# Optimization experiments

Hardware: AMD Instinct MI355X
Metric: run time of the kernel (lower is better)

The kernel has to match this reference:

```python
import jax, jax.numpy as jnp
import numpy as np

VOCAB = 32000
HIDDEN = 1024


def setup_inputs() -> dict:
    key = jax.random.key(0)
    k1, k2, k3 = jax.random.split(key, 3)
    inputs = jax.random.randint(k1, (4, 4096), 0, VOCAB, dtype=jnp.int64 if jax.config.jax_enable_x64 else jnp.int32)
    W0 = jax.random.normal(k2, (VOCAB, 2 * HIDDEN), dtype=jnp.float32)
    W1 = jax.random.normal(k3, (2 * HIDDEN, HIDDEN), dtype=jnp.float32)
    return {"inputs": inputs, "W0": W0, "W1": W1}


def reference(inputs, W0, W1):
    # Original builds one-hot [N, V] and does two GEMMs; mathematically this is
    # a gather of W0 rows followed by a matmul with W1.
    x = W0[inputs]                      # [B, L, 2H]  (== one_hot @ W0)
    emb = jnp.einsum('blk,kh->blh', x, W1)  # [B, L, H]
    mask = (inputs != 0).astype(emb.dtype)  # zero out padding token 0
    emb = emb * mask[..., None]
    emb = emb * jnp.asarray(HIDDEN ** 0.5, emb.dtype)
    return emb
```

## Files before the change

kernel.cpp:

```cpp
#include <hip/hip_runtime.h>
#include <stdint.h>

#define VOCAB 32000
#define KDIM  2048
#define NDIM  1024
#define MTOK  16384

typedef __bf16 bf16x8  __attribute__((ext_vector_type(8)));
typedef float  f32x4   __attribute__((ext_vector_type(4)));
typedef float  f32x16  __attribute__((ext_vector_type(16)));

__device__ __forceinline__ uint32_t pkbf(float a, float b) {
    union { __bf16 h[2]; uint32_t u; } r;
    r.h[0] = (__bf16)a; r.h[1] = (__bf16)b;
    return r.u;
}

__device__ __forceinline__ unsigned short f2bf(float f) {
    union { float f; uint32_t u; } v; v.f = f;
    uint32_t u = v.u;
    return (unsigned short)((u + 0x7FFFu + ((u >> 16) & 1u)) >> 16);
}

__device__ __forceinline__ void gload_lds16(const void* g, void* l) {
    __builtin_amdgcn_global_load_lds(
        (const __attribute__((address_space(1))) uint32_t*)g,
        (__attribute__((address_space(3))) uint32_t*)l,
        16, 0, 0);
}

__global__ void w1_transpose_kernel(const float* __restrict__ W1,
                                    unsigned short* __restrict__ W1T) {
    __shared__ unsigned short tile[32][33];
    const int k0 = blockIdx.x * 32;
    const int n0 = blockIdx.y * 32;
    const int tx = threadIdx.x;
    const int ty = threadIdx.y;
#pragma unroll
    for (int i = 0; i < 4; ++i) {
        int kl = ty + i * 8;
        tile[kl][tx] = __builtin_bit_cast(unsigned short,
                            (__bf16)W1[(size_t)(k0 + kl) * NDIM + n0 + tx]);
    }
    __syncthreads();
#pragma unroll
    for (int i = 0; i < 4; ++i) {
        int nl = ty + i * 8;
        W1T[(size_t)(n0 + nl) * KDIM + k0 + tx] = tile[tx][nl];
    }
}

__global__ __launch_bounds__(512, 2)
void emb_gemm_ws(const int* __restrict__ idx,
                 const float* __restrict__ W0,
                 const unsigned short* __restrict__ W1T,
                 float* __restrict__ out) {
    __shared__ __align__(16) char Abuf[2][256 * 128];
    __shared__ __align__(16) char Bbuf[2][256 * 128];

    const int tid  = threadIdx.x;
    const int lane = tid & 63;
    const int wav  = tid >> 6;
    const int wm   = wav >> 2;
    const int wn   = wav & 3;
    const int m0   = blockIdx.x * 256;
    const int n0   = blockIdx.y * 256;

    const int ac = tid & 15;
    uint32_t aoff[8];
    int abyte[8];
#pragma unroll
    for (int it = 0; it < 8; ++it) {
        const int r = (tid >> 4) + it * 32;
        aoff[it]  = ((uint32_t)idx[m0 + r] * KDIM + ac * 4) * 4u;
        abyte[it] = (r * 128 + ac * 8) ^ ((r & 7) << 4);
    }

    const int brin = lane >> 3;
    const int bch  = (lane & 7) ^ brin;
    uint32_t boff[4];
    int bbase[4];
#pragma unroll
    for (int i = 0; i < 4; ++i) {
        const int rg = wav * 32 + i * 8;
        boff[i]  = ((uint32_t)(n0 + rg + brin) * KDIM + bch * 8) * 2u;
        bbase[i] = rg * 128;
    }

    f32x4  apre[8];
    f32x16 acc[4][2] = {};
    bf16x8 bfv[2];

#define ISSUE_A(t)                                                   \
    _Pragma("unroll")                                                \
    for (int it = 0; it < 8; ++it)                                   \
        apre[it] = *(const f32x4*)((const char*)W0 + aoff[it] + (t) * 256);

#define WRITE_A(buf)                                                 \
    _Pragma("unroll")                                                \
    for (int it = 0; it < 8; ++it) {                                 \
        uint2 pk;                                                    \
        pk.x = pkbf(apre[it][0], apre[it][1]);                       \
        pk.y = pkbf(apre[it][2], apre[it][3]);                       \
        *(uint2*)(Abuf[buf] + abyte[it]) = pk;                       \
    }

#define ISSUE_B(buf, t)                                              \
    _Pragma("unroll")                                                \
    for (int i = 0; i < 4; ++i)                                      \
        gload_lds16((const char*)W1T + boff[i] + (t) * 128,          \
                    Bbuf[buf] + bbase[i]);

    const int rl31 = lane & 31;
    const int khi  = (lane >> 5) * 16;

#define READ_AB(buf, ks, af)                                         \
    _Pragma("unroll")                                                \
    for (int mb = 0; mb < 4; ++mb) {                                 \
        const int r = wm * 128 + mb * 32 + rl31;                     \
        af[mb] = *(const bf16x8*)(Abuf[buf] +                        \
            ((r * 128 + (ks) * 32 + khi) ^ ((r & 7) << 4)));         \
    }                                                                \
    _Pragma("unroll")                                                \
    for (int nb = 0; nb < 2; ++nb) {                                 \
        const int n = wn * 64 + nb * 32 + rl31;                      \
        bfv[nb] = *(const bf16x8*)(Bbuf[buf] +                       \
            ((n * 128 + (ks) * 32 + khi) ^ ((n & 7) << 4)));         \
    }

#define MFMA8(af)                                                    \
    __builtin_amdgcn_s_setprio(1);                                   \
    _Pragma("unroll")                                                \
    for (int mb = 0; mb < 4; ++mb)                                   \
        _Pragma("unroll")                                            \
        for (int nb = 0; nb < 2; ++nb)                               \
            acc[mb][nb] = __builtin_amdgcn_mfma_f32_32x32x16_bf16(   \
                af[mb], bfv[nb], acc[mb][nb], 0, 0, 0);              \
    __builtin_amdgcn_s_setprio(0);

    ISSUE_B(0, 0);
    ISSUE_A(0);
    WRITE_A(0);
    __syncthreads();

    for (int t = 0; t < 32; ++t) {
        const int cur = t & 1, nxt = cur ^ 1;
        const bool pf = (t < 31);
        bf16x8 af[4];

        READ_AB(cur, 0, af);
        if (pf) { ISSUE_B(nxt, t + 1); ISSUE_A(t + 1); }
        __builtin_amdgcn_s_barrier();
        MFMA8(af);
        __builtin_amdgcn_s_barrier();

        READ_AB(cur, 1, af);
        __builtin_amdgcn_s_barrier();
        MFMA8(af);
        __builtin_amdgcn_s_barrier();

        READ_AB(cur, 2, af);
        __builtin_amdgcn_s_barrier();
        MFMA8(af);
        __builtin_amdgcn_s_barrier();

        READ_AB(cur, 3, af);
        if (pf) { WRITE_A(nxt); }
        __builtin_amdgcn_s_barrier();
        MFMA8(af);
        __syncthreads();
    }

    const int hi4 = (lane >> 5) * 4;
#pragma unroll
    for (int mb = 0; mb < 4; ++mb) {
#pragma unroll
        for (int q = 0; q < 4; ++q) {
#pragma unroll
            for (int rs = 0; rs < 4; ++rs) {
                const int reg = q * 4 + rs;
                const int m = m0 + wm * 128 + mb * 32 + q * 8 + rs + hi4;
                const float msk = (idx[m] != 0) ? 32.0f : 0.0f;
#pragma unroll
                for (int nb = 0; nb < 2; ++nb) {
                    const int n = n0 + wn * 64 + nb * 32 + rl31;
                    out[(size_t)m * NDIM + n] = acc[mb][nb][reg] * msk;
                }
            }
        }
    }
#undef ISSUE_A
#undef WRITE_A
#undef ISSUE_B
#undef READ_AB
#undef MFMA8
}

__global__ __launch_bounds__(256)
void emb_gemm_nows(const int* __restrict__ idx,
                   const float* __restrict__ W0,
                   const float* __restrict__ W1,
                   float* __restrict__ out) {
    __shared__ __align__(16) char A_lds[128 * 128];
    __shared__ __align__(16) char B_lds[128 * 128];

    const int tid  = threadIdx.x;
    const int lane = tid & 63;
    const int wav  = tid >> 6;
    const int wm = wav >> 1;
    const int wn = wav & 1;
    const int m0 = blockIdx.x * 128;
    const int n0 = blockIdx.y * 128;

    const float* aSrc[8];
    int arow[8];
#pragma unroll
    for (int it = 0; it < 8; ++it) {
        int r = it * 16 + (tid >> 4);
        arow[it] = r;
        aSrc[it] = W0 + (size_t)idx[m0 + r] * KDIM;
    }
    const int acol4 = tid & 15;

    f32x4 acc[4][4] = {};

    for (int k0 = 0; k0 < KDIM; k0 += 64) {
#pragma unroll
        for (int it = 0; it < 8; ++it) {
            const int r = arow[it];
            const float4 v = *(const float4*)(aSrc[it] + k0 + acol4 * 4);
            uint2 pk;
            pk.x = pkbf(v.x, v.y);
            pk.y = pkbf(v.z, v.w);
            *(uint2*)(A_lds + ((r * 128 + acol4 * 8) ^ ((r & 7) << 4))) = pk;
        }
#pragma unroll
        for (int it = 0; it < 8; ++it) {
            const int k  = it * 8 + (tid >> 5);
            const int n4 = (tid & 31) * 4;
            const float4 v = *(const float4*)(W1 + (size_t)(k0 + k) * NDIM + n0 + n4);
            unsigned short h[4] = { f2bf(v.x), f2bf(v.y), f2bf(v.z), f2bf(v.w) };
#pragma unroll
            for (int i = 0; i < 4; ++i) {
                const int n = n4 + i;
                *(unsigned short*)(B_lds + ((n * 128 + k * 2) ^ ((n & 7) << 4))) = h[i];
            }
        }
        __syncthreads();

#pragma unroll
        for (int ks = 0; ks < 2; ++ks) {
            const int kb = ks * 64 + (lane >> 4) * 16;
            bf16x8 af[4], bfv[4];
#pragma unroll
            for (int mi = 0; mi < 4; ++mi) {
                const int r = wm * 64 + mi * 16 + (lane & 15);
                af[mi] = *(const bf16x8*)(A_lds + ((r * 128 + kb) ^ ((r & 7) << 4)));
            }
#pragma unroll
            for (int ni = 0; ni < 4; ++ni) {
                const int n = wn * 64 + ni * 16 + (lane & 15);
                bfv[ni] = *(const bf16x8*)(B_lds + ((n * 128 + kb) ^ ((n & 7) << 4)));
            }
#pragma unroll
            for (int mi = 0; mi < 4; ++mi)
#pragma unroll
                for (int ni = 0; ni < 4; ++ni)
                    acc[mi][ni] = __builtin_amdgcn_mfma_f32_16x16x32_bf16(
                        af[mi], bfv[ni], acc[mi][ni], 0, 0, 0);
        }
        __syncthreads();
    }

    const int col  = lane & 15;
    const int rowq = (lane >> 4) * 4;
#pragma unroll
    for (int mi = 0; mi < 4; ++mi) {
#pragma unroll
        for (int r = 0; r < 4; ++r) {
            const int m = m0 + wm * 64 + mi * 16 + rowq + r;
            const float msk = (idx[m] != 0) ? 32.0f : 0.0f;
#pragma unroll
            for (int ni = 0; ni < 4; ++ni) {
                const int n = n0 + wn * 64 + ni * 16 + col;
                out[(size_t)m * NDIM + n] = acc[mi][ni][r] * msk;
            }
        }
    }
}

extern "C" void kernel_launch(void* const* d_in, const int* in_sizes, int n_in,
                              void* d_out, int out_size, void* d_ws, size_t ws_size,
                              hipStream_t stream) {
    const int*   idx = (const int*)d_in[0];
    const float* W0  = (const float*)d_in[1];
    const float* W1  = (const float*)d_in[2];
    float*       out = (float*)d_out;

    const size_t w1t_bytes = (size_t)KDIM * NDIM * 2;

    if (ws_size >= w1t_bytes) {
        unsigned short* W1T = (unsigned short*)d_ws;
        dim3 tgrid(KDIM / 32, NDIM / 32);
        w1_transpose_kernel<<<tgrid, dim3(32, 8), 0, stream>>>(W1, W1T);
        dim3 grid(MTOK / 256, NDIM / 256);
        emb_gemm_ws<<<grid, 512, 0, stream>>>(idx, W0, W1T, out);
    } else {
        dim3 grid(MTOK / 128, NDIM / 128);
        emb_gemm_nows<<<grid, 256, 0, stream>>>(idx, W0, W1, out);
    }
}
```

Measured before the change: 101.2 us.

## Switch to 16x16x32 MFMA with register double-buffered LDS fragment reads

Replaces the 32x32x16 MFMA tiling with 16x16x32 bf16 MFMAs arranged as an 8x4 accumulator grid per wave, splitting each K-tile into two 64-wide K steps and two M halves. Fragment reads from LDS are ping-ponged between two register sets so the next set loads while the current MFMAs run, and the next tile's first fragments are prefetched after the barrier. This aims to hide LDS read latency and cut the number of barrier phases per tile, at the cost of more fragment registers and a changed epilogue layout.

```diff
diff --git a/kernel.cpp b/kernel.cpp
--- a/kernel.cpp
+++ b/kernel.cpp
@@ -6,9 +6,8 @@
 #define NDIM  1024
 #define MTOK  16384
 
-typedef __bf16 bf16x8  __attribute__((ext_vector_type(8)));
-typedef float  f32x4   __attribute__((ext_vector_type(4)));
-typedef float  f32x16  __attribute__((ext_vector_type(16)));
+typedef __bf16 bf16x8 __attribute__((ext_vector_type(8)));
+typedef float  f32x4  __attribute__((ext_vector_type(4)));
 
 __device__ __forceinline__ uint32_t pkbf(float a, float b) {
     union { __bf16 h[2]; uint32_t u; } r;
@@ -87,9 +86,12 @@
         bbase[i] = rg * 128;
     }
 
-    f32x4  apre[8];
-    f32x16 acc[4][2] = {};
-    bf16x8 bfv[2];
+    f32x4 apre[8];
+    f32x4 acc[8][4] = {};
+    bf16x8 afX[4], afY[4], bfX[4], bfY[4];
+
+    const int rl = lane & 15;
+    const int kq = (lane >> 4) * 16;
 
 #define ISSUE_A(t)                                                   \
     _Pragma("unroll")                                                \
@@ -111,89 +113,90 @@
         gload_lds16((const char*)W1T + boff[i] + (t) * 128,          \
                     Bbuf[buf] + bbase[i]);
 
-    const int rl31 = lane & 31;
-    const int khi  = (lane >> 5) * 16;
-
-#define READ_AB(buf, ks, af)                                         \
-    _Pragma("unroll")                                                \
-    for (int mb = 0; mb < 4; ++mb) {                                 \
-        const int r = wm * 128 + mb * 32 + rl31;                     \
-        af[mb] = *(const bf16x8*)(Abuf[buf] +                        \
-            ((r * 128 + (ks) * 32 + khi) ^ ((r & 7) << 4)));         \
-    }                                                                \
-    _Pragma("unroll")                                                \
-    for (int nb = 0; nb < 2; ++nb) {                                 \
-        const int n = wn * 64 + nb * 32 + rl31;                      \
-        bfv[nb] = *(const bf16x8*)(Bbuf[buf] +                       \
-            ((n * 128 + (ks) * 32 + khi) ^ ((n & 7) << 4)));         \
-    }
-
-#define MFMA8(af)                                                    \
+#define READ_A(buf, ks, mh, dst)                                     \
+    _Pragma("unroll")                                                \
+    for (int mi = 0; mi < 4; ++mi) {                                 \
+        const int r = wm * 128 + (mh) * 64 + mi * 16 + rl;           \
+        dst[mi] = *(const bf16x8*)(Abuf[buf] +                       \
+            ((r * 128 + (ks) * 64 + kq) ^ ((r & 7) << 4)));          \
+    }
+
+#define READ_B(buf, ks, dst)                                         \
+    _Pragma("unroll")                                                \
+    for (int ni = 0; ni < 4; ++ni) {                                 \
+        const int n = wn * 64 + ni * 16 + rl;                        \
+        dst[ni] = *(const bf16x8*)(Bbuf[buf] +                       \
+            ((n * 128 + (ks) * 64 + kq) ^ ((n & 7) << 4)));          \
+    }
+
+#define MFMA16(af, bf, mh)                                           \
     __builtin_amdgcn_s_setprio(1);                                   \
     _Pragma("unroll")                                                \
-    for (int mb = 0; mb < 4; ++mb)                                   \
+    for (int mi = 0; mi < 4; ++mi)                                   \
         _Pragma("unroll")                                            \
-        for (int nb = 0; nb < 2; ++nb)                               \
-            acc[mb][nb] = __builtin_amdgcn_mfma_f32_32x32x16_bf16(   \
-                af[mb], bfv[nb], acc[mb][nb], 0, 0, 0);              \
+        for (int ni = 0; ni < 4; ++ni)                               \
+            acc[(mh) * 4 + mi][ni] =                                 \
+                __builtin_amdgcn_mfma_f32_16x16x32_bf16(             \
+                    af[mi], bf[ni], acc[(mh) * 4 + mi][ni], 0, 0, 0);\
     __builtin_amdgcn_s_setprio(0);
 
     ISSUE_B(0, 0);
     ISSUE_A(0);
     WRITE_A(0);
     __syncthreads();
+    READ_A(0, 0, 0, afX);
+    READ_B(0, 0, bfX);
 
     for (int t = 0; t < 32; ++t) {
         const int cur = t & 1, nxt = cur ^ 1;
         const bool pf = (t < 31);
-        bf16x8 af[4];
-
-        READ_AB(cur, 0, af);
+
         if (pf) { ISSUE_B(nxt, t + 1); ISSUE_A(t + 1); }
-        __builtin_amdgcn_s_barrier();
-        MFMA8(af);
-        __builtin_amdgcn_s_barrier();
-
-        READ_AB(cur, 1, af);
-        __builtin_amdgcn_s_barrier();
-        MFMA8(af);
-        __builtin_amdgcn_s_barrier();
-
-        READ_AB(cur, 2, af);
-        __builtin_amdgcn_s_barrier();
-        MFMA8(af);
-        __builtin_amdgcn_s_barrier();
-
-        READ_AB(cur, 3, af);
+        READ_A(cur, 0, 1, afY);
+        __builtin_amdgcn_s_barrier();
+        MFMA16(afX, bfX, 0);
+        __builtin_amdgcn_s_barrier();
+
+        READ_A(cur, 1, 0, afX);
+        READ_B(cur, 1, bfY);
+        __builtin_amdgcn_s_barrier();
+        MFMA16(afY, bfX, 1);
+        __builtin_amdgcn_s_barrier();
+
+        READ_A(cur, 1, 1, afY);
+        __builtin_amdgcn_s_barrier();
+        MFMA16(afX, bfY, 0);
+        __builtin_amdgcn_s_barrier();
+
         if (pf) { WRITE_A(nxt); }
-        __builtin_amdgcn_s_barrier();
-        MFMA8(af);
         __syncthreads();
-    }
-
-    const int hi4 = (lane >> 5) * 4;
-#pragma unroll
-    for (int mb = 0; mb < 4; ++mb) {
-#pragma unroll
-        for (int q = 0; q < 4; ++q) {
-#pragma unroll
-            for (int rs = 0; rs < 4; ++rs) {
-                const int reg = q * 4 + rs;
-                const int m = m0 + wm * 128 + mb * 32 + q * 8 + rs + hi4;
-                const float msk = (idx[m] != 0) ? 32.0f : 0.0f;
-#pragma unroll
-                for (int nb = 0; nb < 2; ++nb) {
-                    const int n = n0 + wn * 64 + nb * 32 + rl31;
-                    out[(size_t)m * NDIM + n] = acc[mb][nb][reg] * msk;
-                }
+        if (pf) {
+            READ_A(nxt, 0, 0, afX);
+            READ_B(nxt, 0, bfX);
+        }
+        MFMA16(afY, bfY, 1);
+    }
+
+    const int rowq = (lane >> 4) * 4;
+#pragma unroll
+    for (int mi = 0; mi < 8; ++mi) {
+#pragma unroll
+        for (int r = 0; r < 4; ++r) {
+            const int m = m0 + wm * 128 + mi * 16 + rowq + r;
+            const float msk = (idx[m] != 0) ? 32.0f : 0.0f;
+#pragma unroll
+            for (int ni = 0; ni < 4; ++ni) {
+                const int n = n0 + wn * 64 + ni * 16 + rl;
+                out[(size_t)m * NDIM + n] = acc[mi][ni][r] * msk;
             }
         }
     }
 #undef ISSUE_A
 #undef WRITE_A
 #undef ISSUE_B
-#undef READ_AB
-#undef MFMA8
+#undef READ_A
+#undef READ_B
+#undef MFMA16
 }
 
 __global__ __launch_bounds__(256)
```

Result: slower. 264.2 us (+161.2%).
